# Performance work log

Hardware: AMD Instinct MI355X
Metric: run time of the kernel (lower is better)

The kernel has to match this reference:

```python
import jax, jax.numpy as jnp
import numpy as np
from jax import lax

L = 2048        # leaves per tree
VOCAB = 50000
IN_DIM = 300
MEM = 150
HID = 50
NCLS = 5


def _balanced_tree(n_leaf):
    # children-before-parent topological order; node ids: [0, n_leaf) leaves,
    # [n_leaf, 2*n_leaf-1) internal, last id is the root's single child (ROOT is passthrough).
    level = list(range(n_leaf)); nid = n_leaf; lefts = []; rights = []
    while len(level) > 1:
        nxt = []
        for j in range(0, len(level) - 1, 2):
            lefts.append(level[j]); rights.append(level[j + 1]); nxt.append(nid); nid += 1
        if len(level) % 2:
            nxt.append(level[-1])
        level = nxt
    return np.asarray(lefts, np.int32), np.asarray(rights, np.int32)


def setup_inputs() -> dict:
    key = jax.random.key(0)
    ks = jax.random.split(key, 12)
    left, right = _balanced_tree(L)
    s = 0.05
    return {
        "l_tokens": jax.random.randint(ks[0], (L,), 0, VOCAB, dtype=jnp.int32),
        "r_tokens": jax.random.randint(ks[1], (L,), 0, VOCAB, dtype=jnp.int32),
        "left_idx": jnp.asarray(left),
        "right_idx": jnp.asarray(right),
        "emb": jax.random.normal(ks[2], (VOCAB, IN_DIM), jnp.float32) * s,
        "W_ioux": jax.random.normal(ks[3], (IN_DIM, 3 * MEM), jnp.float32) * s,
        "b_ioux": jnp.zeros((3 * MEM,), jnp.float32),
        "W_iouh": jax.random.normal(ks[4], (MEM, 3 * MEM), jnp.float32) * s,
        "b_iouh": jnp.zeros((3 * MEM,), jnp.float32),
        "W_fx": jax.random.normal(ks[5], (IN_DIM, MEM), jnp.float32) * s,
        "b_fx": jnp.zeros((MEM,), jnp.float32),
        "W_fh": jax.random.normal(ks[6], (MEM, MEM), jnp.float32) * s,
        "b_fh": jnp.zeros((MEM,), jnp.float32),
        "W_attn": jax.random.normal(ks[7], (2 * MEM, MEM), jnp.float32) * s,
        "b_attn": jnp.zeros((MEM,), jnp.float32),
        "W_wh": jax.random.normal(ks[8], (2 * MEM, HID), jnp.float32) * s,
        "b_wh": jnp.zeros((HID,), jnp.float32),
        "W_wp": jax.random.normal(ks[9], (HID, NCLS), jnp.float32) * s,
        "b_wp": jnp.zeros((NCLS,), jnp.float32),
    }


def _gates(iou):
    i, o, u = jnp.split(iou, 3, axis=-1)
    return jax.nn.sigmoid(i), jax.nn.sigmoid(o), jnp.tanh(u)


def _tree_lstm(tokens, left, right, emb, W_ioux, b_ioux, W_iouh, b_iouh, W_fh, b_fh):
    # Leaves (child_c = child_h = 0): iou = ioux(x) + iouh(0); fc term vanishes.
    x = emb[tokens]                                   # [L, in_dim]
    i, o, u = _gates(x @ W_ioux + b_ioux + b_iouh)
    c_leaf = i * u
    h_leaf = o * jnp.tanh(c_leaf)
    n_leaf = tokens.shape[0]
    N = 2 * n_leaf - 1
    C = jnp.zeros((N, MEM), x.dtype).at[:n_leaf].set(c_leaf)
    H = jnp.zeros((N, MEM), x.dtype).at[:n_leaf].set(h_leaf)

    # Internal nodes (inputs=None branch): iou = iouh(sum h_child); f_k = sigmoid(fh(h_k)).
    def step(carry, inp):
        C, H = carry
        k, li, ri = inp
        hl, hr = H[li], H[ri]
        i, o, u = _gates((hl + hr) @ W_iouh + b_iouh)
        fl = jax.nn.sigmoid(hl @ W_fh + b_fh)
        fr = jax.nn.sigmoid(hr @ W_fh + b_fh)
        c = i * u + fl * C[li] + fr * C[ri]
        h = o * jnp.tanh(c)
        return (C.at[k].set(c), H.at[k].set(h)), None

    ids = jnp.arange(n_leaf, N, dtype=jnp.int32)
    (C, H), _ = lax.scan(step, (C, H), (ids, left, right))
    return H  # [N, MEM]; H[-1] is the root hidden state (ROOT is passthrough)


def reference(l_tokens, r_tokens, left_idx, right_idx, emb, W_ioux, b_ioux, W_iouh, b_iouh, W_fx, b_fx, W_fh, b_fh, W_attn, b_attn, W_wh, b_wh, W_wp, b_wp):
    Hl = _tree_lstm(l_tokens, left_idx, right_idx, emb, W_ioux, b_ioux, W_iouh, b_iouh, W_fh, b_fh)
    Hr = _tree_lstm(r_tokens, left_idx, right_idx, emb, W_ioux, b_ioux, W_iouh, b_iouh, W_fh, b_fh)
    # Soft cross-attention over all node hidden states (torch code builds [Nr,Nl,m] beta;
    # here expressed as matmuls -- identical math).
    scores = Hl @ Hr.T                               # [Nl, Nr]
    beta_sum = jax.nn.softmax(scores, axis=1) @ Hr    # [Nl, MEM]
    alpha_sum = jax.nn.softmax(scores.T, axis=1) @ Hl  # [Nr, MEM]
    v_l = jnp.concatenate([Hl, beta_sum], axis=1) @ W_attn + b_attn
    v_r = jnp.concatenate([Hr, alpha_sum], axis=1) @ W_attn + b_attn
    lh = v_l[-1:]  # root hidden (root_idx is the root's matched row)
    rh = v_r[-1:]
    feats = jnp.concatenate([lh * rh, jnp.abs(lh - rh)], axis=1)
    hid = jax.nn.sigmoid(feats @ W_wh + b_wh)
    return jax.nn.log_softmax(hid @ W_wp + b_wp, axis=-1)  # [1, NCLS]
```

## Files before the change

### kernel.cpp

```cpp
#include <hip/hip_runtime.h>
#include <math.h>

#define LEAVES 2048
#define NN     4095
#define MEMD   150
#define IOUD   450
#define IND    300
#define STR    152
#define CT     4096
#define NT     29
#define KT     10
#define IOUSTR 464

__device__ __forceinline__ float sigf(float x) { return 1.f / (1.f + expf(-x)); }

__device__ __forceinline__ unsigned short f2bf(float v) {
    union { float f; unsigned u; } x; x.f = v;
    unsigned r = x.u + 0x7fffu + ((x.u >> 16) & 1u);
    return (unsigned short)(r >> 16);
}

typedef short bf16x8 __attribute__((ext_vector_type(8)));
typedef float f32x4  __attribute__((ext_vector_type(4)));

__global__ __launch_bounds__(256) void k_pack2(
    const float* __restrict__ Wh, const float* __restrict__ Wf,
    const float* __restrict__ Wx,
    float4* __restrict__ PWhf, unsigned short* __restrict__ PB)
{
    int i = blockIdx.x * 256 + threadIdx.x;
    if (i < 22500) {
        int k = i / 150, d = i - k * 150;
        float4 v;
        v.x = Wh[k * IOUD + d];
        v.y = Wh[k * IOUD + 150 + d];
        v.z = Wh[k * IOUD + 300 + d];
        v.w = Wf[k * MEMD + d];
        PWhf[i] = v;
    } else if (i < 22500 + NT * KT * 64) {
        int j2 = i - 22500;
        int nt = j2 / (KT * 64);
        int rem = j2 - nt * (KT * 64);
        int kt = rem >> 6, l = rem & 63;
        int jc = nt * 16 + (l & 15);
        int kb = kt * 32 + ((l >> 4) << 3);
        unsigned short o[8];
        #pragma unroll
        for (int e = 0; e < 8; ++e) {
            int k = kb + e;
            float v = (k < IND && jc < IOUD) ? Wx[k * IOUD + jc] : 0.f;
            o[e] = f2bf(v);
        }
        *(ushort4*)(PB + (size_t)j2 * 8)     = make_ushort4(o[0], o[1], o[2], o[3]);
        *(ushort4*)(PB + (size_t)j2 * 8 + 4) = make_ushort4(o[4], o[5], o[6], o[7]);
    }
}

__global__ __launch_bounds__(256) void k_prepx(
    const int* __restrict__ ltok, const int* __restrict__ rtok,
    const float* __restrict__ emb, unsigned short* __restrict__ Xb)
{
    int idx = blockIdx.x * 256 + threadIdx.x;
    if (idx >= 4096 * 80) return;
    int row = idx / 80, q = idx - row * 80;
    int kb = q * 4;
    int leaf = row & 2047, tree = row >> 11;
    int tk = (tree ? rtok : ltok)[leaf];
    unsigned short o[4];
    #pragma unroll
    for (int e = 0; e < 4; ++e) {
        int k = kb + e;
        float v = (k < IND) ? emb[(size_t)tk * IND + k] : 0.f;
        o[e] = f2bf(v);
    }
    *(ushort4*)(Xb + (size_t)row * 320 + kb) = make_ushort4(o[0], o[1], o[2], o[3]);
}

__global__ __launch_bounds__(256) void k_gemm(
    const unsigned short* __restrict__ Xb, const unsigned short* __restrict__ PB,
    float* __restrict__ IOU)
{
    const int wave = threadIdx.x >> 6, l = threadIdx.x & 63;
    const int tid = blockIdx.x * 4 + wave;
    const int mt = tid / NT, nt = tid - mt * NT;

    const short* Ap = (const short*)Xb + (size_t)(mt * 16 + (l & 15)) * 320 + ((l >> 4) << 3);
    const short* Bp = (const short*)PB + (size_t)nt * (KT * 512) + l * 8;

    f32x4 acc = {0.f, 0.f, 0.f, 0.f};
    #pragma unroll
    for (int kt = 0; kt < KT; ++kt) {
        bf16x8 a = *(const bf16x8*)(Ap + kt * 32);
        bf16x8 b = *(const bf16x8*)(Bp + kt * 512);
        acc = __builtin_amdgcn_mfma_f32_16x16x32_bf16(a, b, acc, 0, 0, 0);
    }

    const int col = nt * 16 + (l & 15);
    const int rb  = mt * 16 + ((l >> 4) << 2);
    #pragma unroll
    for (int r = 0; r < 4; ++r)
        IOU[(size_t)(rb + r) * IOUSTR + col] = acc[r];
}

__global__ __launch_bounds__(256) void k_act(
    const float* __restrict__ IOU,
    const float* __restrict__ bx, const float* __restrict__ bh,
    float* __restrict__ C, float* __restrict__ H)
{
    int idx = blockIdx.x * 256 + threadIdx.x;
    if (idx >= 4096 * 150) return;
    int m = idx / 150, d = idx - m * 150;
    const float* r = IOU + (size_t)m * IOUSTR;
    float iv = r[d]       + bx[d]       + bh[d];
    float ov = r[d + 150] + bx[d + 150] + bh[d + 150];
    float uv = r[d + 300] + bx[d + 300] + bh[d + 300];
    float c = sigf(iv) * tanhf(uv);
    float h = sigf(ov) * tanhf(c);
    int tree = m >> 11, leaf = m & 2047;
    C[((size_t)tree * CT + leaf) * STR + d] = c;
    H[((size_t)tree * CT + leaf) * STR + d] = h;
}

__global__ __launch_bounds__(640) void k_lvl(
    const float4* __restrict__ PWhf, const float* __restrict__ bh,
    const float* __restrict__ bf,
    float* __restrict__ C, float* __restrict__ H, int PB_, int CB)
{
    __shared__ float buf[MEMD][8];
    __shared__ float pb[300][11];
    const int tree = blockIdx.y, t = threadIdx.x;
    const int p0 = blockIdx.x * 4;
    float* Ct = C + (size_t)tree * CT * STR;
    float* Ht = H + (size_t)tree * CT * STR;

    if (t < 600) {
        int m = t / 150, d2 = t - m * 150;
        int cc = CB + 2 * (p0 + m);
        float a = Ht[(size_t)cc * STR + d2];
        float b = Ht[(size_t)(cc + 1) * STR + d2];
        buf[d2][2*m + 0] = a + b;
        buf[d2][2*m + 1] = a;
    }
    __syncthreads();

    const int kh = (t >= 320) ? 1 : 0;
    const int tt = t - 320 * kh;
    const bool act = (tt < 300);
    const int hf = (tt >= 150) ? 1 : 0;
    const int d  = tt - 150 * hf;
    const int m0 = hf * 2;

    float ai[2], ao[2], au[2], afs[2], afl[2], cl[2], cr[2];
    if (act) {
        if (kh == 0) {
            const float bi = bh[d], bo = bh[d + 150], bu = bh[d + 300], bfv = bf[d];
            #pragma unroll
            for (int m = 0; m < 2; ++m) {
                ai[m] = bi; ao[m] = bo; au[m] = bu;
                afs[m] = 2.f * bfv; afl[m] = bfv;
                int cc = CB + 2 * (p0 + m0 + m);
                cl[m] = Ct[(size_t)cc * STR + d];
                cr[m] = Ct[(size_t)(cc + 1) * STR + d];
            }
        } else {
            #pragma unroll
            for (int m = 0; m < 2; ++m) {
                ai[m] = 0.f; ao[m] = 0.f; au[m] = 0.f; afs[m] = 0.f; afl[m] = 0.f;
            }
        }
        const float4* wp = PWhf + d;
        const int kb = kh * 75;
        #pragma unroll 5
        for (int kk = 0; kk < 75; ++kk) {
            const int k = kb + kk;
            float4 w = wp[(size_t)k * 150];
            float4 p4 = *(const float4*)(&buf[k][2 * m0]);
            float hs0 = p4.x, hl0 = p4.y, hs1 = p4.z, hl1 = p4.w;
            ai[0]  = fmaf(hs0, w.x, ai[0]);   ai[1]  = fmaf(hs1, w.x, ai[1]);
            ao[0]  = fmaf(hs0, w.y, ao[0]);   ao[1]  = fmaf(hs1, w.y, ao[1]);
            au[0]  = fmaf(hs0, w.z, au[0]);   au[1]  = fmaf(hs1, w.z, au[1]);
            afs[0] = fmaf(hs0, w.w, afs[0]);  afs[1] = fmaf(hs1, w.w, afs[1]);
            afl[0] = fmaf(hl0, w.w, afl[0]);  afl[1] = fmaf(hl1, w.w, afl[1]);
        }
    }
    if (kh == 1 && act) {
        #pragma unroll
        for (int m = 0; m < 2; ++m) {
            pb[tt][5*m + 0] = ai[m];
            pb[tt][5*m + 1] = ao[m];
            pb[tt][5*m + 2] = au[m];
            pb[tt][5*m + 3] = afs[m];
            pb[tt][5*m + 4] = afl[m];
        }
    }
    __syncthreads();
    if (kh == 0 && act) {
        #pragma unroll
        for (int m = 0; m < 2; ++m) {
            float aiv  = ai[m]  + pb[tt][5*m + 0];
            float aov  = ao[m]  + pb[tt][5*m + 1];
            float auv  = au[m]  + pb[tt][5*m + 2];
            float afsv = afs[m] + pb[tt][5*m + 3];
            float aflv = afl[m] + pb[tt][5*m + 4];
            float frv = afsv - aflv;
            float c = sigf(aiv) * tanhf(auv) + sigf(aflv) * cl[m] + sigf(frv) * cr[m];
            float h = sigf(aov) * tanhf(c);
            size_t rw = (size_t)(PB_ + p0 + m0 + m) * STR + d;
            Ct[rw] = c;
            Ht[rw] = h;
        }
    }
}

__global__ __launch_bounds__(640) void k_node(
    const float4* __restrict__ PWhf, const float* __restrict__ bh,
    const float* __restrict__ bf,
    float* __restrict__ C, float* __restrict__ H, int PB_, int CB)
{
    __shared__ float hsv[MEMD], hlv[MEMD];
    __shared__ float part[4][5][152];
    const int tree = blockIdx.y, node = blockIdx.x, t = threadIdx.x;
    float* Ct = C + (size_t)tree * CT * STR;
    float* Ht = H + (size_t)tree * CT * STR;
    const int c0 = CB + 2 * node;

    if (t < MEMD) {
        float a = Ht[(size_t)c0 * STR + t];
        float b = Ht[(size_t)(c0 + 1) * STR + t];
        hsv[t] = a + b;
        hlv[t] = a;
    }
    __syncthreads();

    const int grp = t / 160, d = t - grp * 160;
    if (d < MEMD) {
        const int k0 = (grp * MEMD) >> 2;
        const int k1 = ((grp + 1) * MEMD) >> 2;
        float ai = 0.f, ao = 0.f, au = 0.f, afs = 0.f, afl = 0.f;
        const float4* wp = PWhf + d;
        #pragma unroll 4
        for (int k = k0; k < k1; ++k) {
            float4 w = wp[(size_t)k * 150];
            float hs = hsv[k], hl = hlv[k];
            ai  = fmaf(hs, w.x, ai);
            ao  = fmaf(hs, w.y, ao);
            au  = fmaf(hs, w.z, au);
            afs = fmaf(hs, w.w, afs);
            afl = fmaf(hl, w.w, afl);
        }
        part[grp][0][d] = ai;  part[grp][1][d] = ao;  part[grp][2][d] = au;
        part[grp][3][d] = afs; part[grp][4][d] = afl;
    }
    __syncthreads();

    if (t < MEMD) {
        const int d2 = t;
        float ai = bh[d2], ao = bh[d2 + 150], au = bh[d2 + 300];
        float bfv = bf[d2];
        float afs = 2.f * bfv, afl = bfv;
        #pragma unroll
        for (int g = 0; g < 4; ++g) {
            ai  += part[g][0][d2]; ao  += part[g][1][d2]; au += part[g][2][d2];
            afs += part[g][3][d2]; afl += part[g][4][d2];
        }
        float cl = Ct[(size_t)c0 * STR + d2];
        float cr = Ct[(size_t)(c0 + 1) * STR + d2];
        float frv = afs - afl;
        float c = sigf(ai) * tanhf(au) + sigf(afl) * cl + sigf(frv) * cr;
        float h = sigf(ao) * tanhf(c);
        size_t rw = (size_t)(PB_ + node) * STR + d2;
        Ct[rw] = c;
        Ht[rw] = h;
    }
}

__global__ __launch_bounds__(256) void k_attn(
    const float* __restrict__ H, float* __restrict__ cstat, float* __restrict__ part)
{
    __shared__ float lv[MEMD];
    __shared__ float sc[64];
    __shared__ float pv[64];
    const int bid = blockIdx.x, t = threadIdx.x;
    const int side = bid >> 6, chunk = bid & 63;
    const int j0 = chunk << 6;
    const int jn = min(64, NN - j0);
    const float* lastrow = H + ((size_t)side * CT + (NN - 1)) * STR;
    if (t < MEMD) lv[t] = lastrow[t];
    __syncthreads();

    const float* src = H + (size_t)(side ^ 1) * CT * STR + (size_t)j0 * STR;
    const int wave = t >> 6, lane = t & 63;
    for (int r = wave; r < jn; r += 4) {
        const float* row = src + (size_t)r * STR;
        float a = lv[lane] * row[lane] + lv[lane + 64] * row[lane + 64];
        if (lane < 22) a += lv[lane + 128] * row[lane + 128];
        #pragma unroll
        for (int off = 32; off; off >>= 1) a += __shfl_xor(a, off);
        if (lane == 0) sc[r] = a;
    }
    __syncthreads();
    if (wave == 0) {
        float v = (lane < jn) ? sc[lane] : -3.4e38f;
        float m = v;
        #pragma unroll
        for (int off = 32; off; off >>= 1) m = fmaxf(m, __shfl_xor(m, off));
        float e = (lane < jn) ? expf(v - m) : 0.f;
        pv[lane] = e;
        float s = e;
        #pragma unroll
        for (int off = 32; off; off >>= 1) s += __shfl_xor(s, off);
        if (lane == 0) {
            cstat[(side * 64 + chunk) * 2 + 0] = m;
            cstat[(side * 64 + chunk) * 2 + 1] = s;
        }
    }
    __syncthreads();
    if (t < MEMD) {
        float a = 0.f;
        for (int j = 0; j < jn; ++j) a += pv[j] * src[(size_t)j * STR + t];
        part[(size_t)(side * 64 + chunk) * STR + t] = a;
    }
}

__global__ __launch_bounds__(512) void k_final(
    const float* __restrict__ H, const float* __restrict__ cstat,
    const float* __restrict__ part,
    const float* __restrict__ Wattn, const float* __restrict__ battn,
    const float* __restrict__ Wwh, const float* __restrict__ bwh,
    const float* __restrict__ Wwp, const float* __restrict__ bwp,
    float* __restrict__ outp)
{
    __shared__ float scl[2][64];
    __shared__ float gseS[2];
    __shared__ float ba[300], catl[300], catr[300], vl[150], vr[150];
    __shared__ float feats[300], hid[50], logits[5];
    const int t = threadIdx.x, wave = t >> 6, lane = t & 63;

    if (wave < 2) {
        float lm = cstat[(wave * 64 + lane) * 2 + 0];
        float ls = cstat[(wave * 64 + lane) * 2 + 1];
        float m = lm;
        #pragma unroll
        for (int off = 32; off; off >>= 1) m = fmaxf(m, __shfl_xor(m, off));
        float s = expf(lm - m);
        scl[wave][lane] = s;
        float se = ls * s;
        #pragma unroll
        for (int off = 32; off; off >>= 1) se += __shfl_xor(se, off);
        if (lane == 0) gseS[wave] = se;
    }
    __syncthreads();
    if (t < 300) {
        int side = t / MEMD, d = t - side * MEMD;
        float a = 0.f;
        for (int c = 0; c < 64; ++c)
            a += part[(size_t)(side * 64 + c) * STR + d] * scl[side][c];
        ba[t] = a / gseS[side];
    }
    __syncthreads();
    const float* Hl_last = H + (size_t)(0 * CT + NN - 1) * STR;
    const float* Hr_last = H + (size_t)(1 * CT + NN - 1) * STR;
    if (t < MEMD) {
        catl[t] = Hl_last[t]; catl[150 + t] = ba[t];
        catr[t] = Hr_last[t]; catr[150 + t] = ba[150 + t];
    }
    __syncthreads();
    if (t < 300) {
        int d = (t < 150) ? t : t - 150;
        const float* cat = (t < 150) ? catl : catr;
        float a = battn[d];
        for (int k = 0; k < 300; ++k) a = fmaf(cat[k], Wattn[k * 150 + d], a);
        if (t < 150) vl[d] = a; else vr[d] = a;
    }
    __syncthreads();
    if (t < MEMD) {
        feats[t] = vl[t] * vr[t];
        feats[150 + t] = fabsf(vl[t] - vr[t]);
    }
    __syncthreads();
    if (t < 50) {
        float a = bwh[t];
        for (int k = 0; k < 300; ++k) a = fmaf(feats[k], Wwh[k * 50 + t], a);
        hid[t] = sigf(a);
    }
    __syncthreads();
    if (t < 5) {
        float a = bwp[t];
        for (int g = 0; g < 50; ++g) a = fmaf(hid[g], Wwp[g * 5 + t], a);
        logits[t] = a;
    }
    __syncthreads();
    if (t == 0) {
        float m = logits[0];
        for (int c = 1; c < 5; ++c) m = fmaxf(m, logits[c]);
        float s = 0.f;
        for (int c = 0; c < 5; ++c) s += expf(logits[c] - m);
        float lse = m + logf(s);
        for (int c = 0; c < 5; ++c) outp[c] = logits[c] - lse;
    }
}

extern "C" void kernel_launch(void* const* d_in, const int* in_sizes, int n_in,
                              void* d_out, int out_size, void* d_ws, size_t ws_size,
                              hipStream_t stream)
{
    const int*   ltok  = (const int*)d_in[0];
    const int*   rtok  = (const int*)d_in[1];
    const float* emb   = (const float*)d_in[4];
    const float* Wx    = (const float*)d_in[5];
    const float* bx    = (const float*)d_in[6];
    const float* Wh    = (const float*)d_in[7];
    const float* bh    = (const float*)d_in[8];
    const float* Wf    = (const float*)d_in[11];
    const float* bf    = (const float*)d_in[12];
    const float* Wattn = (const float*)d_in[13];
    const float* battn = (const float*)d_in[14];
    const float* Wwh   = (const float*)d_in[15];
    const float* bwh   = (const float*)d_in[16];
    const float* Wwp   = (const float*)d_in[17];
    const float* bwp   = (const float*)d_in[18];
    float* out = (float*)d_out;

    float* ws    = (float*)d_ws;
    float*  C    = ws;
    float*  H    = C + (size_t)2 * CT * STR;
    float*  cs   = H + (size_t)2 * CT * STR;
    float*  part = cs + 256;
    float4* PWhf = (float4*)(part + (size_t)128 * STR);
    float*  IOU  = (float*)(PWhf + 22500);
    unsigned short* Xb = (unsigned short*)(IOU + (size_t)4096 * IOUSTR);
    unsigned short* PBb = Xb + (size_t)4096 * 320;

    k_pack2<<<dim3(161), dim3(256), 0, stream>>>(Wh, Wf, Wx, PWhf, PBb);
    k_prepx<<<dim3(1280), dim3(256), 0, stream>>>(ltok, rtok, emb, Xb);
    k_gemm<<<dim3(256 * NT / 4), dim3(256), 0, stream>>>(Xb, PBb, IOU);
    k_act<<<dim3(2400), dim3(256), 0, stream>>>(IOU, bx, bh, C, H);

    k_lvl<<<dim3(256, 2), dim3(640), 0, stream>>>(PWhf, bh, bf, C, H, 2048, 0);
    k_lvl<<<dim3(128, 2), dim3(640), 0, stream>>>(PWhf, bh, bf, C, H, 3072, 2048);
    k_lvl<<<dim3(64,  2), dim3(640), 0, stream>>>(PWhf, bh, bf, C, H, 3584, 3072);

    k_node<<<dim3(128, 2), dim3(640), 0, stream>>>(PWhf, bh, bf, C, H, 3840, 3584);
    k_node<<<dim3(64,  2), dim3(640), 0, stream>>>(PWhf, bh, bf, C, H, 3968, 3840);
    k_node<<<dim3(32,  2), dim3(640), 0, stream>>>(PWhf, bh, bf, C, H, 4032, 3968);
    k_node<<<dim3(16,  2), dim3(640), 0, stream>>>(PWhf, bh, bf, C, H, 4064, 4032);
    k_node<<<dim3(8,   2), dim3(640), 0, stream>>>(PWhf, bh, bf, C, H, 4080, 4064);
    k_node<<<dim3(4,   2), dim3(640), 0, stream>>>(PWhf, bh, bf, C, H, 4088, 4080);
    k_node<<<dim3(2,   2), dim3(640), 0, stream>>>(PWhf, bh, bf, C, H, 4092, 4088);
    k_node<<<dim3(1,   2), dim3(640), 0, stream>>>(PWhf, bh, bf, C, H, 4094, 4092);

    k_attn<<<dim3(128), dim3(256), 0, stream>>>(H, cs, part);
    k_final<<<dim3(1), dim3(512), 0, stream>>>(H, cs, part, Wattn, battn,
                                               Wwh, bwh, Wwp, bwp, out);
}
```

Baseline: 143.8 us.

## Replace fp32 level kernels with bf16 MFMA GEMM plus separate activation pass

The three widest tree levels were computed by fp32 FMA kernels that each reloaded the packed recurrent weights for four parents. They are now a bf16 MFMA GEMM over the children's summed and left hidden states (both trees batched) against a prepacked Wh|Wf matrix, followed by an elementwise gate/activation kernel. This is meant to cut FMA and weight-load cost, at the price of bf16 precision in the recurrence, an extra launch per level, and a round trip of the intermediate through global memory.

```diff
diff --git a/kernel.cpp b/kernel.cpp
--- a/kernel.cpp
+++ b/kernel.cpp
@@ -11,6 +11,10 @@
 #define NT     29
 #define KT     10
 #define IOUSTR 464
+#define KT5    5
+#define NTW    39
+#define LTILES 49
+#define OUTSTR 784
 
 __device__ __forceinline__ float sigf(float x) { return 1.f / (1.f + expf(-x)); }
 
@@ -26,7 +30,8 @@
 __global__ __launch_bounds__(256) void k_pack2(
     const float* __restrict__ Wh, const float* __restrict__ Wf,
     const float* __restrict__ Wx,
-    float4* __restrict__ PWhf, unsigned short* __restrict__ PB)
+    float4* __restrict__ PWhf, unsigned short* __restrict__ PB,
+    unsigned short* __restrict__ PBW)
 {
     int i = blockIdx.x * 256 + threadIdx.x;
     if (i < 22500) {
@@ -53,6 +58,26 @@
         }
         *(ushort4*)(PB + (size_t)j2 * 8)     = make_ushort4(o[0], o[1], o[2], o[3]);
         *(ushort4*)(PB + (size_t)j2 * 8 + 4) = make_ushort4(o[4], o[5], o[6], o[7]);
+    } else if (i < 22500 + NT * KT * 64 + NTW * KT5 * 64) {
+        int j3 = i - 22500 - NT * KT * 64;
+        int bt = j3 / (KT5 * 64);
+        int rem = j3 - bt * (KT5 * 64);
+        int kt = rem >> 6, l = rem & 63;
+        int jc = bt * 16 + (l & 15);
+        int kb = kt * 32 + ((l >> 4) << 3);
+        unsigned short o[8];
+        #pragma unroll
+        for (int e = 0; e < 8; ++e) {
+            int k = kb + e;
+            float v = 0.f;
+            if (k < MEMD) {
+                if (jc < IOUD)                 v = Wh[k * IOUD + jc];
+                else if (jc >= 464 && jc < 614) v = Wf[k * MEMD + (jc - 464)];
+            }
+            o[e] = f2bf(v);
+        }
+        *(ushort4*)(PBW + (size_t)j3 * 8)     = make_ushort4(o[0], o[1], o[2], o[3]);
+        *(ushort4*)(PBW + (size_t)j3 * 8 + 4) = make_ushort4(o[4], o[5], o[6], o[7]);
     }
 }
 
@@ -121,95 +146,101 @@
     H[((size_t)tree * CT + leaf) * STR + d] = h;
 }
 
-__global__ __launch_bounds__(640) void k_lvl(
-    const float4* __restrict__ PWhf, const float* __restrict__ bh,
-    const float* __restrict__ bf,
-    float* __restrict__ C, float* __restrict__ H, int PB_, int CB)
-{
-    __shared__ float buf[MEMD][8];
-    __shared__ float pb[300][11];
-    const int tree = blockIdx.y, t = threadIdx.x;
-    const int p0 = blockIdx.x * 4;
-    float* Ct = C + (size_t)tree * CT * STR;
-    float* Ht = H + (size_t)tree * CT * STR;
-
-    if (t < 600) {
-        int m = t / 150, d2 = t - m * 150;
-        int cc = CB + 2 * (p0 + m);
-        float a = Ht[(size_t)cc * STR + d2];
-        float b = Ht[(size_t)(cc + 1) * STR + d2];
-        buf[d2][2*m + 0] = a + b;
-        buf[d2][2*m + 1] = a;
-    }
-    __syncthreads();
-
-    const int kh = (t >= 320) ? 1 : 0;
-    const int tt = t - 320 * kh;
-    const bool act = (tt < 300);
-    const int hf = (tt >= 150) ? 1 : 0;
-    const int d  = tt - 150 * hf;
-    const int m0 = hf * 2;
-
-    float ai[2], ao[2], au[2], afs[2], afl[2], cl[2], cr[2];
-    if (act) {
-        if (kh == 0) {
-            const float bi = bh[d], bo = bh[d + 150], bu = bh[d + 300], bfv = bf[d];
+__global__ __launch_bounds__(256) void k_lvlg(
+    const unsigned short* __restrict__ PBW,
+    const float* __restrict__ H, float* __restrict__ OUT,
+    int n, int CB)
+{
+    __shared__ unsigned short AS[KT5 * 64 * 8];
+    __shared__ unsigned short AL[KT5 * 64 * 8];
+    const int t = threadIdx.x;
+    const int m0 = blockIdx.x * 16;
+
+    for (int s = t; s < KT5 * 64; s += 256) {
+        int kt = s >> 6, l = s & 63;
+        int m = m0 + (l & 15);
+        int tree = (m >= n) ? 1 : 0;
+        int p = m - tree * n;
+        const float* rL = H + ((size_t)tree * CT + (CB + 2 * p)) * STR;
+        const float* rR = rL + STR;
+        int kb = kt * 32 + ((l >> 4) << 3);
+        unsigned short hs8[8], hl8[8];
+        if (kb + 8 <= MEMD) {
+            float4 a0 = *(const float4*)(rL + kb);
+            float4 a1 = *(const float4*)(rL + kb + 4);
+            float4 b0 = *(const float4*)(rR + kb);
+            float4 b1 = *(const float4*)(rR + kb + 4);
+            float av[8] = {a0.x,a0.y,a0.z,a0.w,a1.x,a1.y,a1.z,a1.w};
+            float bv[8] = {b0.x,b0.y,b0.z,b0.w,b1.x,b1.y,b1.z,b1.w};
             #pragma unroll
-            for (int m = 0; m < 2; ++m) {
-                ai[m] = bi; ao[m] = bo; au[m] = bu;
-                afs[m] = 2.f * bfv; afl[m] = bfv;
-                int cc = CB + 2 * (p0 + m0 + m);
-                cl[m] = Ct[(size_t)cc * STR + d];
-                cr[m] = Ct[(size_t)(cc + 1) * STR + d];
+            for (int e = 0; e < 8; ++e) {
+                hs8[e] = f2bf(av[e] + bv[e]);
+                hl8[e] = f2bf(av[e]);
             }
         } else {
             #pragma unroll
-            for (int m = 0; m < 2; ++m) {
-                ai[m] = 0.f; ao[m] = 0.f; au[m] = 0.f; afs[m] = 0.f; afl[m] = 0.f;
+            for (int e = 0; e < 8; ++e) {
+                int k = kb + e;
+                float a = (k < MEMD) ? rL[k] : 0.f;
+                float b = (k < MEMD) ? rR[k] : 0.f;
+                hs8[e] = f2bf(a + b);
+                hl8[e] = f2bf(a);
             }
         }
-        const float4* wp = PWhf + d;
-        const int kb = kh * 75;
-        #pragma unroll 5
-        for (int kk = 0; kk < 75; ++kk) {
-            const int k = kb + kk;
-            float4 w = wp[(size_t)k * 150];
-            float4 p4 = *(const float4*)(&buf[k][2 * m0]);
-            float hs0 = p4.x, hl0 = p4.y, hs1 = p4.z, hl1 = p4.w;
-            ai[0]  = fmaf(hs0, w.x, ai[0]);   ai[1]  = fmaf(hs1, w.x, ai[1]);
-            ao[0]  = fmaf(hs0, w.y, ao[0]);   ao[1]  = fmaf(hs1, w.y, ao[1]);
-            au[0]  = fmaf(hs0, w.z, au[0]);   au[1]  = fmaf(hs1, w.z, au[1]);
-            afs[0] = fmaf(hs0, w.w, afs[0]);  afs[1] = fmaf(hs1, w.w, afs[1]);
-            afl[0] = fmaf(hl0, w.w, afl[0]);  afl[1] = fmaf(hl1, w.w, afl[1]);
-        }
-    }
-    if (kh == 1 && act) {
-        #pragma unroll
-        for (int m = 0; m < 2; ++m) {
-            pb[tt][5*m + 0] = ai[m];
-            pb[tt][5*m + 1] = ao[m];
-            pb[tt][5*m + 2] = au[m];
-            pb[tt][5*m + 3] = afs[m];
-            pb[tt][5*m + 4] = afl[m];
-        }
-    }
-    __syncthreads();
-    if (kh == 0 && act) {
-        #pragma unroll
-        for (int m = 0; m < 2; ++m) {
-            float aiv  = ai[m]  + pb[tt][5*m + 0];
-            float aov  = ao[m]  + pb[tt][5*m + 1];
-            float auv  = au[m]  + pb[tt][5*m + 2];
-            float afsv = afs[m] + pb[tt][5*m + 3];
-            float aflv = afl[m] + pb[tt][5*m + 4];
-            float frv = afsv - aflv;
-            float c = sigf(aiv) * tanhf(auv) + sigf(aflv) * cl[m] + sigf(frv) * cr[m];
-            float h = sigf(aov) * tanhf(c);
-            size_t rw = (size_t)(PB_ + p0 + m0 + m) * STR + d;
-            Ct[rw] = c;
-            Ht[rw] = h;
-        }
-    }
+        *(ushort4*)(AS + (size_t)s * 8)     = make_ushort4(hs8[0], hs8[1], hs8[2], hs8[3]);
+        *(ushort4*)(AS + (size_t)s * 8 + 4) = make_ushort4(hs8[4], hs8[5], hs8[6], hs8[7]);
+        *(ushort4*)(AL + (size_t)s * 8)     = make_ushort4(hl8[0], hl8[1], hl8[2], hl8[3]);
+        *(ushort4*)(AL + (size_t)s * 8 + 4) = make_ushort4(hl8[4], hl8[5], hl8[6], hl8[7]);
+    }
+    __syncthreads();
+
+    const int w = t >> 6, l = t & 63;
+    for (int T = w; T < LTILES; T += 4) {
+        const int isHL = (T >= NTW) ? 1 : 0;
+        const int bT = isHL ? (T - NTW + 29) : T;
+        const unsigned short* As = isHL ? AL : AS;
+        const short* Bp = (const short*)PBW + (size_t)bT * (KT5 * 512) + l * 8;
+        f32x4 acc = {0.f, 0.f, 0.f, 0.f};
+        #pragma unroll
+        for (int kt = 0; kt < KT5; ++kt) {
+            bf16x8 a = *(const bf16x8*)((const short*)As + (kt * 64 + l) * 8);
+            bf16x8 b = *(const bf16x8*)(Bp + kt * 512);
+            acc = __builtin_amdgcn_mfma_f32_16x16x32_bf16(a, b, acc, 0, 0, 0);
+        }
+        const int col = bT * 16 + (l & 15) + (isHL ? 160 : 0);
+        const int rb  = m0 + ((l >> 4) << 2);
+        #pragma unroll
+        for (int r = 0; r < 4; ++r)
+            OUT[(size_t)(rb + r) * OUTSTR + col] = acc[r];
+    }
+}
+
+__global__ __launch_bounds__(256) void k_actL(
+    const float* __restrict__ OUT, const float* __restrict__ bh,
+    const float* __restrict__ bf,
+    float* __restrict__ C, float* __restrict__ H, int n, int PB_, int CB)
+{
+    int idx = blockIdx.x * 256 + threadIdx.x;
+    if (idx >= 2 * n * MEMD) return;
+    int m = idx / MEMD, d = idx - m * MEMD;
+    int tree = (m >= n) ? 1 : 0, p = m - tree * n;
+    const float* R = OUT + (size_t)m * OUTSTR;
+    float* Ct = C + (size_t)tree * CT * STR;
+    float* Ht = H + (size_t)tree * CT * STR;
+    int c0 = CB + 2 * p;
+    float cl = Ct[(size_t)c0 * STR + d];
+    float cr = Ct[(size_t)(c0 + 1) * STR + d];
+    float iv = R[d]       + bh[d];
+    float ov = R[d + 150] + bh[d + 150];
+    float uv = R[d + 300] + bh[d + 300];
+    float fs = R[464 + d] + 2.f * bf[d];
+    float fl = R[624 + d] + bf[d];
+    float fr = fs - fl;
+    float c = sigf(iv) * tanhf(uv) + sigf(fl) * cl + sigf(fr) * cr;
+    float h = sigf(ov) * tanhf(c);
+    size_t rw = (size_t)(PB_ + p) * STR + d;
+    Ct[rw] = c;
+    Ht[rw] = h;
 }
 
 __global__ __launch_bounds__(640) void k_node(
@@ -428,17 +459,22 @@
     float*  part = cs + 256;
     float4* PWhf = (float4*)(part + (size_t)128 * STR);
     float*  IOU  = (float*)(PWhf + 22500);
-    unsigned short* Xb = (unsigned short*)(IOU + (size_t)4096 * IOUSTR);
+    float*  OUT  = IOU + (size_t)4096 * IOUSTR;
+    unsigned short* Xb  = (unsigned short*)(OUT + (size_t)2048 * OUTSTR);
     unsigned short* PBb = Xb + (size_t)4096 * 320;
-
-    k_pack2<<<dim3(161), dim3(256), 0, stream>>>(Wh, Wf, Wx, PWhf, PBb);
+    unsigned short* PBW = PBb + (size_t)NT * KT * 512;
+
+    k_pack2<<<dim3(210), dim3(256), 0, stream>>>(Wh, Wf, Wx, PWhf, PBb, PBW);
     k_prepx<<<dim3(1280), dim3(256), 0, stream>>>(ltok, rtok, emb, Xb);
     k_gemm<<<dim3(256 * NT / 4), dim3(256), 0, stream>>>(Xb, PBb, IOU);
     k_act<<<dim3(2400), dim3(256), 0, stream>>>(IOU, bx, bh, C, H);
 
-    k_lvl<<<dim3(256, 2), dim3(640), 0, stream>>>(PWhf, bh, bf, C, H, 2048, 0);
-    k_lvl<<<dim3(128, 2), dim3(640), 0, stream>>>(PWhf, bh, bf, C, H, 3072, 2048);
-    k_lvl<<<dim3(64,  2), dim3(640), 0, stream>>>(PWhf, bh, bf, C, H, 3584, 3072);
+    k_lvlg<<<dim3(128), dim3(256), 0, stream>>>(PBW, H, OUT, 1024, 0);
+    k_actL<<<dim3(1200), dim3(256), 0, stream>>>(OUT, bh, bf, C, H, 1024, 2048, 0);
+    k_lvlg<<<dim3(64),  dim3(256), 0, stream>>>(PBW, H, OUT, 512, 2048);
+    k_actL<<<dim3(600), dim3(256), 0, stream>>>(OUT, bh, bf, C, H, 512, 3072, 2048);
+    k_lvlg<<<dim3(32),  dim3(256), 0, stream>>>(PBW, H, OUT, 256, 3072);
+    k_actL<<<dim3(300), dim3(256), 0, stream>>>(OUT, bh, bf, C, H, 256, 3584, 3072);
 
     k_node<<<dim3(128, 2), dim3(640), 0, stream>>>(PWhf, bh, bf, C, H, 3840, 3584);
     k_node<<<dim3(64,  2), dim3(640), 0, stream>>>(PWhf, bh, bf, C, H, 3968, 3840);
```

Result: faster. 140.9 us (-2.0%).
